# Performance work log

Measured on AMD Instinct MI355X. Metric: run time of the kernel, lower is better.

## Reference

```python
import jax, jax.numpy as jnp
import numpy as np

ZERO_TOL = 1e-06
KSZ = 3


def setup_inputs() -> dict:
    key = jax.random.key(0)
    k1, k2, k3, k4 = jax.random.split(key, 4)
    B, C, H, W = 8, 3, 64, 64
    NC = 16
    D = 2 * C * KSZ * KSZ  # 54
    x = jax.random.normal(k1, (B, C, H, W), dtype=jnp.float32)
    mask = jax.random.uniform(k2, (NC, D), dtype=jnp.float32, minval=-1.0, maxval=1.0)
    weight = jax.random.uniform(k3, (NC, D), dtype=jnp.float32, minval=0.0, maxval=1.0)
    # module init: bias = mean over channels of weight.sum(1)/2 (constant per channel)
    bias = jnp.full((NC, 1), (weight.sum(1) / 2.0).mean(), dtype=jnp.float32)
    return {"x": x, "mask": mask, "weight": weight, "bias": bias}


def _wos_forward(x, mask, weight, bias):
    B, C, H, W = x.shape
    NC = weight.shape[0]
    # fixed_padding for kernel 3, dilation 1 -> pad 1 on each side ('same')
    xp = jnp.pad(x, ((0, 0), (0, 0), (1, 1), (1, 1)))
    # unfold: torch ordering flattens (C, kh, kw) with C slowest
    patches = jnp.stack(
        [xp[:, :, i:i + H, j:j + W] for i in range(KSZ) for j in range(KSZ)],
        axis=2,
    )  # (B, C, k*k, H, W)
    D0 = C * KSZ * KSZ
    L = H * W
    unf = patches.reshape(B, D0, L)                    # (B, D0, L) like nn.Unfold
    inp = jnp.transpose(unf, (0, 2, 1)).reshape(B * L, 1, D0)  # rows ordered b*L+l
    inp = jnp.concatenate([inp, -inp], axis=2)         # (N, 1, D)
    mx = inp + mask[None]                              # (N, NC, D)
    si = jnp.argsort(-mx, axis=-1)                     # descending sort permutation
    smx = jnp.take_along_axis(mx, si, axis=-1)         # sorted values, descending
    sw = jnp.take_along_axis(jnp.broadcast_to(weight[None], mx.shape), si, axis=-1)
    nz = sw > ZERO_TOL                                 # nonzero-weight positions
    # cumulative sum over the compacted (nonzero) weights, kept in full coords
    accw = jnp.cumsum(jnp.where(nz, sw, 0.0), axis=-1)
    li = jnp.sum(nz & (accw <= bias[None]), axis=-1) - 1   # (N, NC)
    li = jnp.maximum(li, 0)
    # rank among nonzero entries; pick the li-th nonzero sorted value
    rank = jnp.cumsum(nz.astype(jnp.int32), axis=-1) - 1
    sel = nz & (rank == li[..., None])
    y = jnp.sum(jnp.where(sel, smx, 0.0), axis=-1)     # (N, NC)
    # module does result.view(-1, NC, L_sqrt, L_sqrt): raw reinterpret of memory
    return y.reshape(B, NC, H, W)


def reference(x, mask, weight, bias):
    return _wos_forward(x, mask, weight, bias)
```

## Files before the change

kernel.cpp:

```cpp
#include <hip/hip_runtime.h>
#include <limits.h>
#include <math.h>
#include <stdint.h>

#define WOS_ZERO_TOL 1e-6f
#define STRIDE 57

__global__ __launch_bounds__(256) void wos_kernel(
    const float* __restrict__ x,
    const float* __restrict__ mask,
    const float* __restrict__ weight,
    const float* __restrict__ bias,
    float* __restrict__ out)
{
    __shared__ float s_ws[4][16][STRIDE];
    __shared__ float s_mx[4][16][STRIDE];
    __shared__ unsigned long long s_key[4][64];

    const int lane = threadIdx.x & 63;
    const int wid  = threadIdx.x >> 6;
    const int p    = blockIdx.x * 4 + wid;
    const int b    = p >> 12;
    const int l    = p & 4095;
    const int h    = l >> 6;
    const int w    = l & 63;

    float inp = 0.0f;
    if (lane < 54) {
        int dm  = (lane < 27) ? lane : lane - 27;
        int c   = dm / 9;
        int rem = dm - 9 * c;
        int di  = rem / 3;
        int dj  = rem - 3 * di;
        int hh  = h + di - 1;
        int ww  = w + dj - 1;
        if (hh >= 0 && hh < 64 && ww >= 0 && ww < 64) {
            float v = x[((b * 3 + c) << 12) + (hh << 6) + ww];
            inp = (lane < 27) ? v : -v;
        }
    }

    const uint32_t inv_lane = (uint32_t)(63 - lane);

    #pragma unroll 1
    for (int nc = 0; nc < 16; ++nc) {
        float mk   = (lane < 54) ? mask[nc * 54 + lane]   : 0.0f;
        float wv   = (lane < 54) ? weight[nc * 54 + lane] : 0.0f;
        float mxv  = (lane < 54) ? (inp + mk) : -INFINITY;
        float wsel = (wv > WOS_ZERO_TOL) ? wv : 0.0f;

        int      bits = __float_as_int(mxv);
        uint32_t ob   = (uint32_t)(bits ^ ((bits >> 31) | 0x80000000));
        uint64_t myk  = ((uint64_t)ob << 32) | inv_lane;

        s_key[wid][lane] = myk;

        uint32_t rank = 0;
        #pragma unroll
        for (int dp = 0; dp < 54; ++dp) {
            rank += (s_key[wid][dp] > myk) ? 1u : 0u;
        }

        if (lane < 54) {
            s_ws[wid][nc][rank] = wsel;
            s_mx[wid][nc][rank] = mxv;
        }
    }

    {
        const int   nc = lane & 15;
        const float bv = bias[nc];
        float acc   = 0.0f;
        int   rstar = -1;
        int   fnz   = 64;
        #pragma unroll
        for (int r = 0; r < 54; ++r) {
            float wr = s_ws[wid][nc][r];
            acc += wr;
            bool nz = (__float_as_int(wr) != 0);
            rstar = (nz && acc <= bv) ? r : rstar;
            fnz   = (nz && r < fnz)   ? r : fnz;
        }
        if (rstar < 0) rstar = (fnz < 54) ? fnz : 0;
        float ans = s_mx[wid][nc][rstar];
        if (lane < 16) out[p * 16 + lane] = ans;
    }
}

extern "C" void kernel_launch(void* const* d_in, const int* in_sizes, int n_in,
                              void* d_out, int out_size, void* d_ws, size_t ws_size,
                              hipStream_t stream) {
    const float* x      = (const float*)d_in[0];
    const float* mask   = (const float*)d_in[1];
    const float* weight = (const float*)d_in[2];
    const float* bias   = (const float*)d_in[3];
    float* out = (float*)d_out;

    wos_kernel<<<dim3(8192), dim3(256), 0, stream>>>(x, mask, weight, bias, out);
}
```

Measured before the change: 202.2 us.

## Cut LDS footprint, vectorize rank scan, prefetch mask and weight loads

Replaces the per-wave sorted-value shared array with a byte-sized rank table and recovers the selected value in a final pass over the 16 channels, shrinking LDS use to allow more resident blocks (launch bounds now request 8). The rank-counting loop reads keys as 128-bit pairs with two accumulators, and mask and weight loads for the next channel are software-prefetched. The first-nonzero fallback runs only when needed. In exchange it adds an extra loop with mask reloads and reuses key memory for scratch, relying on compiler barriers rather than explicit synchronization within a wave.

```diff
diff --git a/kernel.cpp b/kernel.cpp
--- a/kernel.cpp
+++ b/kernel.cpp
@@ -6,7 +6,7 @@
 #define WOS_ZERO_TOL 1e-6f
 #define STRIDE 57
 
-__global__ __launch_bounds__(256) void wos_kernel(
+__global__ __launch_bounds__(256, 8) void wos_kernel(
     const float* __restrict__ x,
     const float* __restrict__ mask,
     const float* __restrict__ weight,
@@ -14,8 +14,8 @@
     float* __restrict__ out)
 {
     __shared__ float s_ws[4][16][STRIDE];
-    __shared__ float s_mx[4][16][STRIDE];
-    __shared__ unsigned long long s_key[4][64];
+    __shared__ __align__(16) unsigned long long s_key[4][64];
+    __shared__ unsigned char s_rank[4][16][56];
 
     const int lane = threadIdx.x & 63;
     const int wid  = threadIdx.x >> 6;
@@ -41,49 +41,81 @@
     }
 
     const uint32_t inv_lane = (uint32_t)(63 - lane);
+    const int midx = (lane < 54) ? lane : 0;
+
+    float mk_next = mask[midx];
+    float wv_next = weight[midx];
 
     #pragma unroll 1
     for (int nc = 0; nc < 16; ++nc) {
-        float mk   = (lane < 54) ? mask[nc * 54 + lane]   : 0.0f;
-        float wv   = (lane < 54) ? weight[nc * 54 + lane] : 0.0f;
-        float mxv  = (lane < 54) ? (inp + mk) : -INFINITY;
-        float wsel = (wv > WOS_ZERO_TOL) ? wv : 0.0f;
+        const float mk = mk_next;
+        const float wv = wv_next;
+        if (nc < 15) {
+            mk_next = mask[(nc + 1) * 54 + midx];
+            wv_next = weight[(nc + 1) * 54 + midx];
+        }
+        const float mxv  = inp + mk;
+        const float wsel = (wv > WOS_ZERO_TOL) ? wv : 0.0f;
 
-        int      bits = __float_as_int(mxv);
-        uint32_t ob   = (uint32_t)(bits ^ ((bits >> 31) | 0x80000000));
-        uint64_t myk  = ((uint64_t)ob << 32) | inv_lane;
+        const int      bits = __float_as_int(mxv);
+        const uint32_t ob   = (uint32_t)(bits ^ ((bits >> 31) | 0x80000000));
+        const uint64_t myk  = ((uint64_t)ob << 32) | inv_lane;
 
         s_key[wid][lane] = myk;
+        asm volatile("" ::: "memory");
 
-        uint32_t rank = 0;
+        const ulonglong2* kp = (const ulonglong2*)(&s_key[wid][0]);
+        uint32_t r0 = 0, r1 = 0;
         #pragma unroll
-        for (int dp = 0; dp < 54; ++dp) {
-            rank += (s_key[wid][dp] > myk) ? 1u : 0u;
+        for (int i = 0; i < 27; ++i) {
+            ulonglong2 kk = kp[i];
+            r0 += (kk.x > myk) ? 1u : 0u;
+            r1 += (kk.y > myk) ? 1u : 0u;
         }
+        const uint32_t rank = r0 + r1;
 
         if (lane < 54) {
-            s_ws[wid][nc][rank] = wsel;
-            s_mx[wid][nc][rank] = mxv;
+            s_ws[wid][nc][rank]   = wsel;
+            s_rank[wid][nc][lane] = (unsigned char)rank;
         }
     }
 
+    asm volatile("" ::: "memory");
+    int*   s_r   = (int*)(&s_key[wid][0]);
+    float* s_out = (float*)(&s_key[wid][16]);
+
     {
-        const int   nc = lane & 15;
-        const float bv = bias[nc];
+        const int   ncp = lane & 15;
+        const float bv  = bias[ncp];
         float acc   = 0.0f;
         int   rstar = -1;
-        int   fnz   = 64;
         #pragma unroll
         for (int r = 0; r < 54; ++r) {
-            float wr = s_ws[wid][nc][r];
+            float wr = s_ws[wid][ncp][r];
             acc += wr;
-            bool nz = (__float_as_int(wr) != 0);
-            rstar = (nz && acc <= bv) ? r : rstar;
-            fnz   = (nz && r < fnz)   ? r : fnz;
+            rstar = (wr > 0.0f && acc <= bv) ? r : rstar;
         }
-        if (rstar < 0) rstar = (fnz < 54) ? fnz : 0;
-        float ans = s_mx[wid][nc][rstar];
-        if (lane < 16) out[p * 16 + lane] = ans;
+        if (rstar < 0) {
+            #pragma unroll 1
+            for (int r = 53; r >= 0; --r) {
+                float wr = s_ws[wid][ncp][r];
+                rstar = (wr > 0.0f) ? r : rstar;
+            }
+            if (rstar < 0) rstar = 0;
+        }
+        if (lane < 16) s_r[ncp] = rstar;
+    }
+
+    {
+        #pragma unroll 1
+        for (int nc = 0; nc < 16; ++nc) {
+            const int   rk = (int)s_rank[wid][nc][midx];
+            const int   rs = s_r[nc];
+            const float mk = mask[nc * 54 + midx];
+            if (lane < 54 && rk == rs)
+                s_out[nc] = inp + mk;
+        }
+        if (lane < 16) out[p * 16 + lane] = s_out[lane];
     }
 }
 
```

Result: faster. 191.0 us (-5.5%).
